# Optimization experiments

Measured on AMD Instinct MI355X. Metric: run time of the kernel, lower is better.

The kernel has to match this reference:

```python
import jax, jax.numpy as jnp
import numpy as np

NUM_CLASSES = 2
CONF_THRESH = 0.05
NMS_THRESH = 0.3
NMS_TOP_K = 5000
TOP_K = 750
VAR0, VAR1 = 0.1, 0.2
NEG = -1e9  # sentinel for suppressed / below-threshold scores

NUM = 16
PRIORS = 131072


def setup_inputs() -> dict:
    key = jax.random.key(0)
    k1, k2, k3 = jax.random.split(key, 3)
    loc_data = jax.random.normal(k1, (NUM, PRIORS, 4), dtype=jnp.float32)
    conf_data = jax.random.uniform(k2, (NUM * PRIORS, NUM_CLASSES), dtype=jnp.float32)
    prior_data = jax.random.uniform(k3, (PRIORS, 4), dtype=jnp.float32)
    return {"loc_data": loc_data, "conf_data": conf_data, "prior_data": prior_data}


def decode(loc, priors):
    # loc, priors: [N, 4] (cx, cy, w, h priors); SSD box decode -> (x1, y1, x2, y2)
    xy = priors[:, :2] + loc[:, :2] * VAR0 * priors[:, 2:]
    wh = priors[:, 2:] * jnp.exp(loc[:, 2:] * VAR1)
    return jnp.concatenate([xy - wh * 0.5, xy + wh * 0.5], axis=-1)


def _area(b):
    return (b[..., 2] - b[..., 0]) * (b[..., 3] - b[..., 1])


def iou_one_to_many(box, boxes):
    # box: [4], boxes: [K, 4]
    lt = jnp.maximum(box[:2], boxes[:, :2])
    rb = jnp.minimum(box[2:], boxes[:, 2:])
    wh = jnp.clip(rb - lt, 0.0)
    inter = wh[:, 0] * wh[:, 1]
    union = _area(box) + _area(boxes) - inter
    return inter / jnp.maximum(union, 1e-12)


def nms_single(boxes, scores):
    # boxes: [P, 4], scores: [P] (one image, one class) -> [TOP_K, 5] (score, x1, y1, x2, y2)
    s = jnp.where(scores > CONF_THRESH, scores, NEG)
    top_s, top_i = jax.lax.top_k(s, NMS_TOP_K)
    top_b = boxes[top_i]  # [K, 4]
    idx_range = jnp.arange(NMS_TOP_K)

    def step(s_work, _):
        idx = jnp.argmax(s_work)
        sc = s_work[idx]
        valid = sc > NEG * 0.5
        box = top_b[idx]
        ious = iou_one_to_many(box, top_b)
        kill = (ious > NMS_THRESH) | (idx_range == idx)
        s_new = jnp.where(kill, NEG, s_work)
        row = jnp.where(valid, jnp.concatenate([sc[None], box]), jnp.zeros((5,), boxes.dtype))
        return s_new, row

    _, rows = jax.lax.scan(step, top_s, None, length=TOP_K)
    return rows  # [TOP_K, 5]


def reference(loc_data, conf_data, prior_data):
    num, P, _ = loc_data.shape
    conf = conf_data.reshape(num, P, NUM_CLASSES).transpose(0, 2, 1)  # [num, C, P]
    batch_priors = jnp.broadcast_to(prior_data, (num, P, 4)).reshape(-1, 4)
    boxes = decode(loc_data.reshape(-1, 4), batch_priors).reshape(num, P, 4)
    # NMS over non-background classes, vmapped over batch and class
    per_image = jax.vmap(nms_single, in_axes=(None, 0))          # over classes
    det = jax.vmap(per_image)(boxes, conf[:, 1:, :])             # [num, C-1, TOP_K, 5]
    bg = jnp.zeros((num, 1, TOP_K, 5), det.dtype)
    return jnp.concatenate([bg, det], axis=1)                     # [num, C, TOP_K, 5]
```

## Files before the change

### kernel.cpp

```cpp
#include <hip/hip_runtime.h>
#include <cmath>

#pragma clang fp contract(off)

typedef unsigned long long ull;
typedef unsigned int uint;

#define NPRIORS 131072
#define NIMG 16
#define KSEL 5000
#define TOPK 750
#define SORTN 8192
#define MW 80
#define NCHUNK 79
#define KSELP (NCHUNK * 64)
#define NBIN 65536

#define MID03 0.30000002682209014892578125

#define WS_PAIRS 0
#define WS_NDIAG 0
#define WS_MCNT 1048576
#define WS_BOXES 1048832
#define WS_SCORES 2328832
#define WS_MASK 2649088
#define WS_HIST (WS_MASK)
#define WS_CNT  (WS_MASK + 4194304)
#define WS_POS  (WS_MASK + 8388608)
#define WS_DIAG (WS_MASK + (size_t)NIMG * KSEL * MW * 8)

__device__ inline ull readlane64(ull t, int l) {
  unsigned lo = (unsigned)__builtin_amdgcn_readlane((int)(unsigned)t, l);
  unsigned hi = (unsigned)__builtin_amdgcn_readlane((int)(unsigned)(t >> 32), l);
  return ((ull)hi << 32) | lo;
}

__device__ __forceinline__ ull rfl64(ull t) {
  unsigned lo = (unsigned)__builtin_amdgcn_readfirstlane((int)(unsigned)t);
  unsigned hi = (unsigned)__builtin_amdgcn_readfirstlane((int)(unsigned)(t >> 32));
  return ((ull)hi << 32) | lo;
}

__device__ inline void softBarrier() {
  asm volatile("s_waitcnt lgkmcnt(0)\n\ts_barrier" ::: "memory");
}

__device__ __forceinline__ ull kill_mask(const float4 pb, const float pa,
                                         const float4 c, const float ca2) {
  float ltx = fmaxf(pb.x, c.x), lty = fmaxf(pb.y, c.y);
  float rbx = fminf(pb.z, c.z), rby = fminf(pb.w, c.w);
  float ww = fmaxf(rbx - ltx, 0.0f), hh = fmaxf(rby - lty, 0.0f);
  float inter = ww * hh;
  float uni = fmaxf(pa + ca2 - inter, 1e-12f);
  float f = fmaf(-0.3f, uni, inter);
  float band = uni * 0x1p-20f;
  ull wfast = __ballot(f > band);
  ull wamb = __ballot(fabsf(f) <= band);
  if (__builtin_expect(wamb != 0ULL, 0)) {
    asm volatile("" ::: "memory");
    ull wex = __ballot((double)inter > MID03 * (double)uni);
    wfast = (wfast & ~wamb) | (wex & wamb);
  }
  return wfast;
}

__global__ __launch_bounds__(256) void hist_kernel(const float* __restrict__ conf,
                                                   unsigned int* __restrict__ hist) {
  const int img = blockIdx.y;
  const float4* c4 = (const float4*)conf + (size_t)img * (NPRIORS / 2);
  unsigned int* H = hist + (size_t)img * NBIN;
  for (int q = blockIdx.x * 256 + threadIdx.x; q < NPRIORS / 2; q += 64 * 256) {
    float4 v = c4[q];
    if (v.y > 0.05f) atomicAdd(&H[(__float_as_uint(v.y) >> 12) & 0xFFFFu], 1u);
    if (v.w > 0.05f) atomicAdd(&H[(__float_as_uint(v.w) >> 12) & 0xFFFFu], 1u);
  }
}

__global__ __launch_bounds__(1024) void cutoff_kernel(const unsigned int* __restrict__ hist,
                                                      unsigned int* __restrict__ pos,
                                                      int* __restrict__ meta,
                                                      float4* __restrict__ sboxes,
                                                      float* __restrict__ sscores) {
  const int img = blockIdx.x;
  const int tid = threadIdx.x;
  const int lane = tid & 63;
  const int wv = tid >> 6;
  const unsigned int* H = hist + (size_t)img * NBIN;
  unsigned int* P = pos + (size_t)img * NBIN;
  __shared__ unsigned int csum[1024];
  __shared__ unsigned int suf[1024];
  __shared__ int s_cc;
  __shared__ unsigned int s_cut, s_mc;

  for (int g = 0; g < 64; ++g) {
    unsigned int v = H[g * 1024 + tid];
    for (int m = 1; m < 64; m <<= 1) v += __shfl_xor(v, m);
    if (lane == 0) csum[g * 16 + wv] = v;
  }
  __syncthreads();
  suf[tid] = csum[tid];
  if (tid == 0) s_cc = 0;
  __syncthreads();
  for (int off = 1; off < 1024; off <<= 1) {
    unsigned int v = (tid + off < 1024) ? suf[tid + off] : 0u;
    __syncthreads();
    suf[tid] += v;
    __syncthreads();
  }
  if (suf[tid] >= KSEL && (suf[tid] - csum[tid]) < KSEL) s_cc = tid;
  __syncthreads();
  const int cc = s_cc;
  if (tid == 0) { s_cut = (unsigned int)(cc * 64); s_mc = suf[0]; }
  __syncthreads();
  for (int b = cc * 64 + tid; b < NBIN; b += 1024) {
    int q = b >> 6;
    unsigned int acc = (q + 1 < 1024) ? suf[q + 1] : 0u;
    for (int b2 = b + 1; b2 < (q + 1) * 64; ++b2) acc += H[b2];
    P[b] = acc;
    unsigned int h = H[b];
    if (acc < KSEL && acc + h >= KSEL) { s_cut = (unsigned int)b; s_mc = acc + h; }
  }
  __syncthreads();
  if (tid == 0) {
    meta[img] = (int)min(s_mc, (unsigned int)SORTN);
    meta[16 + img] = (int)s_cut;
  }
  for (int i = tid; i < KSEL; i += 1024) {
    sboxes[(size_t)img * KSEL + i] = make_float4(0.f, 0.f, 0.f, 0.f);
    sscores[(size_t)img * KSEL + i] = -1e9f;
  }
}

__global__ __launch_bounds__(256) void scatter_kernel(const float* __restrict__ conf,
                                                      const unsigned int* __restrict__ pos,
                                                      unsigned int* __restrict__ cnt,
                                                      const int* __restrict__ meta,
                                                      ull* __restrict__ pairs) {
  const int img = blockIdx.y;
  const float4* c4 = (const float4*)conf + (size_t)img * (NPRIORS / 2);
  const unsigned int* P = pos + (size_t)img * NBIN;
  unsigned int* Cn = cnt + (size_t)img * NBIN;
  ull* mypairs = pairs + (size_t)img * SORTN;
  const unsigned int cutval = ((unsigned int)meta[16 + img]) << 12;
  for (int q = blockIdx.x * 256 + threadIdx.x; q < NPRIORS / 2; q += 64 * 256) {
    float4 v = c4[q];
#pragma unroll
    for (int h = 0; h < 2; ++h) {
      float sc = h ? v.w : v.y;
      unsigned int p = 2 * (unsigned int)q + h;
      if (sc > 0.05f) {
        unsigned int u = __float_as_uint(sc);
        if (u >= cutval) {
          unsigned int bin = (u >> 12) & 0xFFFFu;
          unsigned int slot = atomicAdd(&Cn[bin], 1u);
          unsigned int idx = P[bin] + slot;
          if (idx < SORTN)
            mypairs[idx] = ((ull)u << 32) | (ull)(0xFFFFFFFFu - p);
        }
      }
    }
  }
}

__global__ __launch_bounds__(256) void rank_decode_kernel(const ull* __restrict__ pairs,
                                                          const unsigned int* __restrict__ hist,
                                                          const unsigned int* __restrict__ pos,
                                                          const int* __restrict__ meta,
                                                          const float* __restrict__ loc,
                                                          const float* __restrict__ prior,
                                                          float4* __restrict__ sboxes,
                                                          float* __restrict__ sscores) {
#pragma clang fp contract(off)
  const int img = blockIdx.y;
  const int s = blockIdx.x * 256 + threadIdx.x;
  const int mc = meta[img];
  if (s >= mc) return;
  const ull* mypairs = pairs + (size_t)img * SORTN;
  const ull key = mypairs[s];
  const unsigned int u = (unsigned int)(key >> 32);
  const unsigned int bin = (u >> 12) & 0xFFFFu;
  const unsigned int base = pos[(size_t)img * NBIN + bin];
  const unsigned int cb = hist[(size_t)img * NBIN + bin];
  const int end = min((int)(base + cb), mc);
  int rank = 0;
  for (int j = (int)base; j < end; ++j) rank += (mypairs[j] > key);
  const int fp = (int)base + rank;
  if (fp >= KSEL) return;
  const unsigned int p = 0xFFFFFFFFu - (unsigned int)(key & 0xFFFFFFFFu);
  const float* lp = loc + ((size_t)img * NPRIORS + p) * 4;
  const float* pp = prior + (size_t)p * 4;
  float l0 = lp[0], l1 = lp[1], l2 = lp[2], l3 = lp[3];
  float px = pp[0], py = pp[1], pw = pp[2], ph = pp[3];
  float cx = px + (l0 * 0.1f) * pw;
  float cy = py + (l1 * 0.1f) * ph;
  float w = pw * (float)exp((double)(l2 * 0.2f));
  float hh = ph * (float)exp((double)(l3 * 0.2f));
  float4 box;
  box.x = cx - w * 0.5f;
  box.y = cy - hh * 0.5f;
  box.z = cx + w * 0.5f;
  box.w = cy + hh * 0.5f;
  sboxes[(size_t)img * KSEL + fp] = box;
  sscores[(size_t)img * KSEL + fp] = __uint_as_float(u);
}

__global__ __launch_bounds__(256) void mask_build_kernel(const float4* __restrict__ sboxes,
                                                         ull* __restrict__ mask,
                                                         ull* __restrict__ diag,
                                                         ull* __restrict__ ndiag) {
#pragma clang fp contract(off)
  const int jt = blockIdx.x;
  const int sp = blockIdx.y;
  const int img = blockIdx.z;
  if (jt < (sp >> 1)) return;
  const int tid = threadIdx.x;
  const int lane = tid & 63;
  const int wave = __builtin_amdgcn_readfirstlane(tid >> 6);
  __shared__ float4 ib[128];
  const float4* bb = sboxes + (size_t)img * KSEL;
  if (tid < 128) {
    int i = sp * 128 + tid;
    ib[tid] = (i < KSEL) ? bb[i] : make_float4(0.f, 0.f, 0.f, 0.f);
  }
  __syncthreads();
  float4 cb[4];
  float ca[4];
#pragma unroll
  for (int s = 0; s < 4; ++s) {
    int j = jt * 256 + s * 64 + lane;
    cb[s] = (j < KSEL) ? bb[j] : make_float4(0.f, 0.f, 0.f, 0.f);
    ca[s] = (cb[s].z - cb[s].x) * (cb[s].w - cb[s].y);
  }
  const int grp0 = jt * 4;
  const int strip = 2 * sp + (wave >> 1);
  const int sd = strip - grp0;
  const int i0 = sp * 128 + wave * 32;
  const int rbase = (wave & 1) * 32;
  const bool needD = (sd >= 0 && sd < 4);
  const bool needN = (sd >= -1 && sd < 3);

  if (i0 < KSEL) {
    uint a0 = 0, a1 = 0, a2 = 0, a3 = 0;
    uint dgl = 0, dgh = 0, ngl = 0, ngh = 0;

#pragma unroll 4
    for (int k = 0; k < 32; ++k) {
      const float4 pb = ib[wave * 32 + k];
      const float pa = (pb.z - pb.x) * (pb.w - pb.y);
      ull w0 = kill_mask(pb, pa, cb[0], ca[0]);
      ull w1 = kill_mask(pb, pa, cb[1], ca[1]);
      ull w2 = kill_mask(pb, pa, cb[2], ca[2]);
      ull w3 = kill_mask(pb, pa, cb[3], ca[3]);
      if (needD) {
        const ull gtm = 0xFFFFFFFFFFFFFFFEULL << (rbase + k);
        ull wd;
        if (sd == 0)      { w0 &= gtm; wd = w0; }
        else if (sd == 1) { w1 &= gtm; wd = w1; }
        else if (sd == 2) { w2 &= gtm; wd = w2; }
        else              { w3 &= gtm; wd = w3; }
        const bool ck = (lane == k);
        dgl = ck ? (uint)wd : dgl;
        dgh = ck ? (uint)(wd >> 32) : dgh;
      }
      if (needN) {
        ull wn;
        if (sd == -1)     wn = w0;
        else if (sd == 0) wn = w1;
        else if (sd == 1) wn = w2;
        else              wn = w3;
        const bool ck = (lane == k);
        ngl = ck ? (uint)wn : ngl;
        ngh = ck ? (uint)(wn >> 32) : ngh;
      }
      const bool c0 = (lane == 2 * k);
      const bool c1 = (lane == 2 * k + 1);
      a0 = c0 ? (uint)w0 : a0;         a0 = c1 ? (uint)w2 : a0;
      a1 = c0 ? (uint)(w0 >> 32) : a1; a1 = c1 ? (uint)(w2 >> 32) : a1;
      a2 = c0 ? (uint)w1 : a2;         a2 = c1 ? (uint)w3 : a2;
      a3 = c0 ? (uint)(w1 >> 32) : a3; a3 = c1 ? (uint)(w3 >> 32) : a3;
    }

    ull* mrow = mask + (size_t)img * KSEL * MW;
    const int row = i0 + (lane >> 1);
    if (row < KSEL) {
      uint* wp = (uint*)(mrow + (size_t)row * MW + grp0) + (lane & 1) * 4;
      *(uint4*)wp = make_uint4(a0, a1, a2, a3);
    }
    const int drow = i0 + lane;
    if (needD && lane < 32 && drow < KSEL)
      diag[(size_t)img * KSELP + drow] = ((ull)dgh << 32) | dgl;
    if (needN && lane < 32 && drow < KSEL)
      ndiag[(size_t)img * KSELP + drow] = ((ull)ngh << 32) | ngl;
  }
}

__global__ __launch_bounds__(128) void sweep_kernel(const ull* __restrict__ mask,
                                                    const ull* __restrict__ diag,
                                                    const ull* __restrict__ ndiag,
                                                    const float4* __restrict__ sboxes,
                                                    const float* __restrict__ sscores,
                                                    const int* __restrict__ meta,
                                                    float* __restrict__ out) {
  const int img = blockIdx.x;
  const int tid = threadIdx.x;
  const int lane = tid & 63;
  const bool waveA = (tid < 64);
  const int V = min(meta[img], KSEL);
  const ull* mb = mask + (size_t)img * KSEL * MW;
  const ull* dg = diag + (size_t)img * KSELP;
  const ull* ng = ndiag + (size_t)img * KSELP;
  __shared__ ull mailbox[NCHUNK + 1];
  __shared__ int pickbuf[TOPK];
  __shared__ int s_np[NCHUNK];
  __shared__ int s_start[NCHUNK];
  __shared__ int s_done;
  __shared__ int s_n;
  const int lc = min(lane, 39);

  for (int i = tid; i <= NCHUNK; i += 128) mailbox[i] = 0ULL;
  if (tid == 0) { s_done = 0; s_n = 0; }
  __syncthreads();

  if (V > 0) {
    ull dw = 0, ndw = 0, dw1 = 0, ndw1 = 0, bridge = 0;
    ull rlo = 0, rhi = 0;
    int nkeep = 0;
    bool adone = false;
    if (waveA) {
      dw = dg[lane]; ndw = ng[lane];
      const int i1 = min(64 + lane, KSELP - 1);
      dw1 = dg[i1]; ndw1 = ng[i1];
    }

    for (int k = 0; k < NCHUNK; ++k) {
      softBarrier();
      if (s_done) break;
      if (waveA) {
        if (!adone) {
          const int base = k * 64;
          const int nidx = min(base + 128 + lane, KSELP - 1);
          ull dw2 = dg[nidx];
          ull ndw2 = ng[nidx];
          ull cur = rfl64(mailbox[k] | bridge);
          bridge = 0ULL;
          const int lim = V - base;
          ull validm = (lim >= 64) ? ~0ULL : ((~0ULL) >> (64 - lim));
          ull avail = (~cur) & validm;
          ull picked = 0ULL;
          const int st = nkeep;
          while (avail != 0ULL && nkeep < TOPK) {
            int r = __builtin_ctzll(avail);
            picked |= (1ULL << r);
            nkeep++;
            ull dr = readlane64(dw, r);
            bridge |= readlane64(ndw, r);
            avail &= ~(dr | (1ULL << r));
          }
          {
            uint plo = (uint)picked, phi = (uint)(picked >> 32);
            int rank = (int)__builtin_amdgcn_mbcnt_hi(
                phi, __builtin_amdgcn_mbcnt_lo(plo, 0u));
            if ((picked >> lane) & 1ULL) pickbuf[st + rank] = base + lane;
          }
          if (lane == 0) { s_np[k] = nkeep - st; s_start[k] = st; }
          if (nkeep >= TOPK || base + 64 >= V) {
            if (lane == 0) { s_done = 1; s_n = (nkeep < TOPK) ? nkeep : TOPK; }
            adone = true;
          }
          dw = dw1; ndw = ndw1;
          dw1 = dw2; ndw1 = ndw2;
        }
      } else if (k >= 1) {
        const int np = s_np[k - 1];
        const int st = s_start[k - 1];
        for (int g = 0; g < np; g += 16) {
          ulonglong2 v[16];
#pragma unroll
          for (int q = 0; q < 16; ++q) {
            int t = min(g + q, np - 1);
            int row = pickbuf[st + t];
            v[q] = *(const ulonglong2*)(mb + (size_t)row * MW + 2 * lc);
          }
#pragma unroll
          for (int q = 0; q < 16; ++q) { rlo |= v[q].x; rhi |= v[q].y; }
        }
        const int w = k + 1;
        if (w < NCHUNK) {
          ull t = (w & 1) ? rhi : rlo;
          ull word = readlane64(t, w >> 1);
          if (lane == 0) mailbox[w] = word;
        }
      }
    }
  }

  __syncthreads();
  const int n = s_n;
  float* ob = out + (size_t)img * (2 * TOPK * 5) + TOPK * 5;
  for (int j = tid; j < n; j += 128) {
    int i = pickbuf[j];
    float4 b = sboxes[(size_t)img * KSEL + i];
    float sc = sscores[(size_t)img * KSEL + i];
    float* o = ob + (size_t)j * 5;
    o[0] = sc; o[1] = b.x; o[2] = b.y; o[3] = b.z; o[4] = b.w;
  }
}

extern "C" void kernel_launch(void* const* d_in, const int* in_sizes, int n_in,
                              void* d_out, int out_size, void* d_ws, size_t ws_size,
                              hipStream_t stream) {
  const float* loc = (const float*)d_in[0];
  const float* conf = (const float*)d_in[1];
  const float* prior = (const float*)d_in[2];
  float* out = (float*)d_out;

  char* ws = (char*)d_ws;
  ull* pairs = (ull*)(ws + WS_PAIRS);
  ull* ndiag = (ull*)(ws + WS_NDIAG);
  int* meta = (int*)(ws + WS_MCNT);
  float4* sboxes = (float4*)(ws + WS_BOXES);
  float* sscores = (float*)(ws + WS_SCORES);
  ull* mask = (ull*)(ws + WS_MASK);
  ull* diag = (ull*)(ws + WS_DIAG);
  unsigned int* hist = (unsigned int*)(ws + WS_HIST);
  unsigned int* cnt = (unsigned int*)(ws + WS_CNT);
  unsigned int* pos = (unsigned int*)(ws + WS_POS);

  hipMemsetAsync(d_out, 0, (size_t)out_size * sizeof(float), stream);
  hipMemsetAsync(ws + WS_HIST, 0, 2u * 4194304u, stream);

  {
    dim3 g(64, NIMG);
    hist_kernel<<<g, 256, 0, stream>>>(conf, hist);
  }
  cutoff_kernel<<<NIMG, 1024, 0, stream>>>(hist, pos, meta, sboxes, sscores);
  {
    dim3 g(64, NIMG);
    scatter_kernel<<<g, 256, 0, stream>>>(conf, pos, cnt, meta, pairs);
  }
  {
    dim3 g((SORTN + 255) / 256, NIMG);
    rank_decode_kernel<<<g, 256, 0, stream>>>(pairs, hist, pos, meta, loc, prior, sboxes, sscores);
  }
  {
    dim3 g(20, 40, NIMG);
    mask_build_kernel<<<g, 256, 0, stream>>>(sboxes, mask, diag, ndiag);
  }
  sweep_kernel<<<NIMG, 128, 0, stream>>>(mask, diag, ndiag, sboxes, sscores, meta, out);
}
```

Measured before the change: 506.0 us.

## Add second-neighbor diagonal mask and software-pipeline mask row loads in sweep

Mask building now also emits a second off-diagonal block (chunk i+2) per row. The sweep's wave A uses it as a two-chunk-ahead bridge, so the mailbox word written by wave B can lag by one more chunk. Wave B now issues the first batch of row loads for chunk k-1 and only ORs them in on the next iteration, hiding global load latency behind the barrier. The cost is extra per-lane state in mask build, another diag array in workspace, and more registers held across iterations in the sweep.

New measurement: 513.2 us. No clear change (+1.4%).

```diff
diff --git a/kernel.cpp b/kernel.cpp
--- a/kernel.cpp
+++ b/kernel.cpp
@@ -28,6 +28,7 @@
 #define WS_CNT  (WS_MASK + 4194304)
 #define WS_POS  (WS_MASK + 8388608)
 #define WS_DIAG (WS_MASK + (size_t)NIMG * KSEL * MW * 8)
+#define WS_N2   (WS_DIAG + (size_t)NIMG * KSELP * 8)
 
 __device__ inline ull readlane64(ull t, int l) {
   unsigned lo = (unsigned)__builtin_amdgcn_readlane((int)(unsigned)t, l);
@@ -207,7 +208,8 @@
 __global__ __launch_bounds__(256) void mask_build_kernel(const float4* __restrict__ sboxes,
                                                          ull* __restrict__ mask,
                                                          ull* __restrict__ diag,
-                                                         ull* __restrict__ ndiag) {
+                                                         ull* __restrict__ ndiag,
+                                                         ull* __restrict__ n2diag) {
 #pragma clang fp contract(off)
   const int jt = blockIdx.x;
   const int sp = blockIdx.y;
@@ -238,10 +240,12 @@
   const int rbase = (wave & 1) * 32;
   const bool needD = (sd >= 0 && sd < 4);
   const bool needN = (sd >= -1 && sd < 3);
+  const bool needN2 = (sd >= -2 && sd < 2);
 
   if (i0 < KSEL) {
     uint a0 = 0, a1 = 0, a2 = 0, a3 = 0;
     uint dgl = 0, dgh = 0, ngl = 0, ngh = 0;
+    uint n2l = 0, n2h = 0;
 
 #pragma unroll 4
     for (int k = 0; k < 32; ++k) {
@@ -272,6 +276,16 @@
         ngl = ck ? (uint)wn : ngl;
         ngh = ck ? (uint)(wn >> 32) : ngh;
       }
+      if (needN2) {
+        ull wn2;
+        if (sd == -2)     wn2 = w0;
+        else if (sd == -1) wn2 = w1;
+        else if (sd == 0)  wn2 = w2;
+        else               wn2 = w3;
+        const bool ck = (lane == k);
+        n2l = ck ? (uint)wn2 : n2l;
+        n2h = ck ? (uint)(wn2 >> 32) : n2h;
+      }
       const bool c0 = (lane == 2 * k);
       const bool c1 = (lane == 2 * k + 1);
       a0 = c0 ? (uint)w0 : a0;         a0 = c1 ? (uint)w2 : a0;
@@ -291,12 +305,15 @@
       diag[(size_t)img * KSELP + drow] = ((ull)dgh << 32) | dgl;
     if (needN && lane < 32 && drow < KSEL)
       ndiag[(size_t)img * KSELP + drow] = ((ull)ngh << 32) | ngl;
+    if (needN2 && lane < 32 && drow < KSEL)
+      n2diag[(size_t)img * KSELP + drow] = ((ull)n2h << 32) | n2l;
   }
 }
 
 __global__ __launch_bounds__(128) void sweep_kernel(const ull* __restrict__ mask,
                                                     const ull* __restrict__ diag,
                                                     const ull* __restrict__ ndiag,
+                                                    const ull* __restrict__ n2diag,
                                                     const float4* __restrict__ sboxes,
                                                     const float* __restrict__ sscores,
                                                     const int* __restrict__ meta,
@@ -309,6 +326,7 @@
   const ull* mb = mask + (size_t)img * KSEL * MW;
   const ull* dg = diag + (size_t)img * KSELP;
   const ull* ng = ndiag + (size_t)img * KSELP;
+  const ull* n2g = n2diag + (size_t)img * KSELP;
   __shared__ ull mailbox[NCHUNK + 1];
   __shared__ int pickbuf[TOPK];
   __shared__ int s_np[NCHUNK];
@@ -322,14 +340,18 @@
   __syncthreads();
 
   if (V > 0) {
-    ull dw = 0, ndw = 0, dw1 = 0, ndw1 = 0, bridge = 0;
+    ull dw = 0, ndw = 0, n2w = 0;
+    ull dw1 = 0, ndw1 = 0, n2w1 = 0;
+    ull brA = 0, brB = 0, pend2 = 0;
     ull rlo = 0, rhi = 0;
+    ulonglong2 vp[16];
+    int npP = 0;
     int nkeep = 0;
     bool adone = false;
     if (waveA) {
-      dw = dg[lane]; ndw = ng[lane];
+      dw = dg[lane]; ndw = ng[lane]; n2w = n2g[lane];
       const int i1 = min(64 + lane, KSELP - 1);
-      dw1 = dg[i1]; ndw1 = ng[i1];
+      dw1 = dg[i1]; ndw1 = ng[i1]; n2w1 = n2g[i1];
     }
 
     for (int k = 0; k < NCHUNK; ++k) {
@@ -341,21 +363,23 @@
           const int nidx = min(base + 128 + lane, KSELP - 1);
           ull dw2 = dg[nidx];
           ull ndw2 = ng[nidx];
-          ull cur = rfl64(mailbox[k] | bridge);
-          bridge = 0ULL;
+          ull n2w2 = n2g[nidx];
+          ull cur = rfl64(mailbox[k]) | brA | brB;
           const int lim = V - base;
           ull validm = (lim >= 64) ? ~0ULL : ((~0ULL) >> (64 - lim));
           ull avail = (~cur) & validm;
-          ull picked = 0ULL;
+          ull picked = 0ULL, aN = 0ULL, aN2 = 0ULL;
           const int st = nkeep;
           while (avail != 0ULL && nkeep < TOPK) {
             int r = __builtin_ctzll(avail);
             picked |= (1ULL << r);
             nkeep++;
             ull dr = readlane64(dw, r);
-            bridge |= readlane64(ndw, r);
+            aN |= readlane64(ndw, r);
+            aN2 |= readlane64(n2w, r);
             avail &= ~(dr | (1ULL << r));
           }
+          brB = pend2; pend2 = aN2; brA = aN;
           {
             uint plo = (uint)picked, phi = (uint)(picked >> 32);
             int rank = (int)__builtin_amdgcn_mbcnt_hi(
@@ -367,22 +391,13 @@
             if (lane == 0) { s_done = 1; s_n = (nkeep < TOPK) ? nkeep : TOPK; }
             adone = true;
           }
-          dw = dw1; ndw = ndw1;
-          dw1 = dw2; ndw1 = ndw2;
+          dw = dw1; ndw = ndw1; n2w = n2w1;
+          dw1 = dw2; ndw1 = ndw2; n2w1 = n2w2;
         }
       } else if (k >= 1) {
-        const int np = s_np[k - 1];
-        const int st = s_start[k - 1];
-        for (int g = 0; g < np; g += 16) {
-          ulonglong2 v[16];
-#pragma unroll
-          for (int q = 0; q < 16; ++q) {
-            int t = min(g + q, np - 1);
-            int row = pickbuf[st + t];
-            v[q] = *(const ulonglong2*)(mb + (size_t)row * MW + 2 * lc);
-          }
-#pragma unroll
-          for (int q = 0; q < 16; ++q) { rlo |= v[q].x; rhi |= v[q].y; }
+        if (npP > 0) {
+#pragma unroll
+          for (int q = 0; q < 16; ++q) { rlo |= vp[q].x; rhi |= vp[q].y; }
         }
         const int w = k + 1;
         if (w < NCHUNK) {
@@ -390,6 +405,28 @@
           ull word = readlane64(t, w >> 1);
           if (lane == 0) mailbox[w] = word;
         }
+        const int np = s_np[k - 1];
+        const int st = s_start[k - 1];
+        if (np > 0) {
+#pragma unroll
+          for (int q = 0; q < 16; ++q) {
+            int t2 = min(q, np - 1);
+            int row = pickbuf[st + t2];
+            vp[q] = *(const ulonglong2*)(mb + (size_t)row * MW + 2 * lc);
+          }
+          for (int g = 16; g < np; g += 16) {
+            ulonglong2 v2[16];
+#pragma unroll
+            for (int q = 0; q < 16; ++q) {
+              int t3 = min(g + q, np - 1);
+              int row = pickbuf[st + t3];
+              v2[q] = *(const ulonglong2*)(mb + (size_t)row * MW + 2 * lc);
+            }
+#pragma unroll
+            for (int q = 0; q < 16; ++q) { rlo |= v2[q].x; rhi |= v2[q].y; }
+          }
+        }
+        npP = np;
       }
     }
   }
@@ -422,6 +459,7 @@
   float* sscores = (float*)(ws + WS_SCORES);
   ull* mask = (ull*)(ws + WS_MASK);
   ull* diag = (ull*)(ws + WS_DIAG);
+  ull* n2diag = (ull*)(ws + WS_N2);
   unsigned int* hist = (unsigned int*)(ws + WS_HIST);
   unsigned int* cnt = (unsigned int*)(ws + WS_CNT);
   unsigned int* pos = (unsigned int*)(ws + WS_POS);
@@ -444,7 +482,7 @@
   }
   {
     dim3 g(20, 40, NIMG);
-    mask_build_kernel<<<g, 256, 0, stream>>>(sboxes, mask, diag, ndiag);
-  }
-  sweep_kernel<<<NIMG, 128, 0, stream>>>(mask, diag, ndiag, sboxes, sscores, meta, out);
-}
+    mask_build_kernel<<<g, 256, 0, stream>>>(sboxes, mask, diag, ndiag, n2diag);
+  }
+  sweep_kernel<<<NIMG, 128, 0, stream>>>(mask, diag, ndiag, n2diag, sboxes, sscores, meta, out);
+}
```
